# Optimization experiments

Measured on AMD Instinct MI355X. Metric: run time of the kernel, lower is better.

## Reference

```python
import jax, jax.numpy as jnp
import numpy as np

B, T = 2, 1024
V, D, H, L = 32000, 1024, 16, 8
DH = D // H  # 64
ROPE_BASE = 1000.0
EPS = 1e-6


def _rms_norm(x):
    # F.rms_norm(x, (C,), eps=1e-6)
    ms = jnp.mean(jnp.square(x), axis=-1, keepdims=True)
    return x * jax.lax.rsqrt(ms + EPS)


def _rope_tables(t_len):
    quarter = DH // 4
    inv_freq = jnp.concatenate([
        ROPE_BASE ** (-jnp.arange(quarter, dtype=jnp.float32) / quarter),
        jnp.zeros(quarter, dtype=jnp.float32),
    ])  # [DH/2]
    theta = jnp.arange(t_len, dtype=jnp.float32)[:, None] * inv_freq[None, :]  # [T, DH/2]
    return jnp.cos(theta), jnp.sin(theta)


def _apply_rope(x, cos, sin):
    # x: [B, H, T, DH]; cos/sin: [T, DH/2] broadcast to [1,1,T,DH/2]
    half = DH // 2
    x1, x2 = x[..., :half], x[..., half:]
    c = cos[None, None]
    s = sin[None, None]
    return jnp.concatenate([c * x1 - s * x2, s * x1 + c * x2], axis=-1).astype(x.dtype)


def setup_inputs() -> dict:
    key = jax.random.key(0)
    ks = jax.random.split(key, 7)
    s = 0.02
    return {
        "x_indices": jax.random.randint(ks[0], (B, T), 0, V, dtype=jnp.int32),
        "embedding": jax.random.normal(ks[1], (V, D), dtype=jnp.float32) * s,
        "Wqkv": jax.random.normal(ks[2], (L, 3 * D, D), dtype=jnp.float32) * s,
        "Wout": jax.random.normal(ks[3], (L, D, D), dtype=jnp.float32) * s,
        "W1": jax.random.normal(ks[4], (L, 4 * D, D), dtype=jnp.float32) * s,
        "W2": jax.random.normal(ks[5], (L, D, 4 * D), dtype=jnp.float32) * s,
        "lm_head": jax.random.normal(ks[6], (V, D), dtype=jnp.float32) * s,
    }


def reference(x_indices, embedding, Wqkv, Wout, W1, W2, lm_head):
    x = embedding[x_indices]  # [B, T, D]
    cos, sin = _rope_tables(T)
    causal = jnp.tril(jnp.ones((T, T), dtype=bool))  # [T, T]
    neg = jnp.finfo(x.dtype).min
    scale = 1.0 / np.sqrt(DH)

    for l in range(L):
        n = _rms_norm(x)
        qkv = jnp.einsum('btd,ed->bte', n, Wqkv[l])  # [B, T, 3D]
        qkv = qkv.reshape(B, T, 3, H, DH)
        q = jnp.transpose(qkv[:, :, 0], (0, 2, 1, 3))  # [B, H, T, DH]
        k = jnp.transpose(qkv[:, :, 1], (0, 2, 1, 3))
        v = jnp.transpose(qkv[:, :, 2], (0, 2, 1, 3))
        q = _apply_rope(q, cos, sin)
        k = _apply_rope(k, cos, sin)
        scores = jnp.einsum('bhqd,bhkd->bhqk', q, k) * scale
        scores = jnp.where(causal[None, None], scores, neg)
        attn = jax.nn.softmax(scores, axis=-1)
        ctx = jnp.einsum('bhqk,bhkd->bhqd', attn, v)
        ctx = jnp.transpose(ctx, (0, 2, 1, 3)).reshape(B, T, D)
        x = x + jnp.einsum('btd,ed->bte', ctx, Wout[l])
        n = _rms_norm(x)
        h = jnp.square(jax.nn.relu(jnp.einsum('btd,fd->btf', n, W1[l])))  # [B, T, 4D]
        x = x + jnp.einsum('btf,df->btd', h, W2[l])

    logits = jnp.einsum('btd,vd->btv', _rms_norm(x), lm_head)
    return logits.astype(jnp.float32)
```

## Files before the change

### kernel.cpp

```cpp
#include <hip/hip_runtime.h>
#include <hip/hip_bf16.h>
#include <cmath>
#include <cstdint>

#define B_  2
#define T_  1024
#define V_  32000
#define D_  1024
#define H_  16
#define L_  8
#define DH_ 64

typedef __attribute__((ext_vector_type(8))) short bf16x8;
typedef __attribute__((ext_vector_type(4))) float f32x4;

__device__ __forceinline__ ushort f2bf(float f) {
    union { float f; uint32_t u; } v; v.f = f;
    uint32_t r = v.u + 0x7FFFu + ((v.u >> 16) & 1u);
    return (ushort)(r >> 16);
}
__device__ __forceinline__ float bf2f(ushort u) {
    union { uint32_t u; float f; } v; v.u = ((uint32_t)u) << 16;
    return v.f;
}

__device__ __forceinline__ void async_copy16(const void* g, void* l) {
    __builtin_amdgcn_global_load_lds(
        (const __attribute__((address_space(1))) void*)g,
        (__attribute__((address_space(3))) void*)l, 16, 0, 0);
}

__global__ __launch_bounds__(256) void k_cast(const float4* __restrict__ in,
                                              ushort4* __restrict__ out, int n4) {
    for (int i = blockIdx.x * 256 + threadIdx.x; i < n4; i += gridDim.x * 256) {
        float4 v = in[i];
        out[i] = make_ushort4(f2bf(v.x), f2bf(v.y), f2bf(v.z), f2bf(v.w));
    }
}

__global__ void k_rope_tables(float* __restrict__ cosT, float* __restrict__ sinT) {
    int t = blockIdx.x;
    int i = threadIdx.x;
    float invf = (i < 16) ? powf(1000.0f, -(float)i / 16.0f) : 0.0f;
    float th = (float)t * invf;
    cosT[t * 32 + i] = cosf(th);
    sinT[t * 32 + i] = sinf(th);
}

__global__ __launch_bounds__(256) void k_gather(const int* __restrict__ idx,
                                                const float* __restrict__ emb,
                                                float* __restrict__ x) {
    int row = blockIdx.x;
    int id = idx[row];
    const float4* src = (const float4*)(emb + (size_t)id * D_);
    float4* dst = (float4*)(x + (size_t)row * D_);
    dst[threadIdx.x] = src[threadIdx.x];
}

__global__ __launch_bounds__(256) void k_rmsnorm(const float* __restrict__ x,
                                                 ushort* __restrict__ out) {
    int row = blockIdx.x;
    const float4* xr = (const float4*)(x + (size_t)row * D_);
    float4 v = xr[threadIdx.x];
    float ss = v.x * v.x + v.y * v.y + v.z * v.z + v.w * v.w;
    #pragma unroll
    for (int off = 1; off < 64; off <<= 1) ss += __shfl_xor(ss, off);
    __shared__ float wsum[4];
    int lane = threadIdx.x & 63, wv = threadIdx.x >> 6;
    if (lane == 0) wsum[wv] = ss;
    __syncthreads();
    float tot = wsum[0] + wsum[1] + wsum[2] + wsum[3];
    float inv = rsqrtf(tot * (1.0f / D_) + 1e-6f);
    ushort4 r = make_ushort4(f2bf(v.x * inv), f2bf(v.y * inv), f2bf(v.z * inv), f2bf(v.w * inv));
    *(ushort4*)(out + (size_t)row * D_ + threadIdx.x * 4) = r;
}

template<int BN, int EPI, bool OUTBF, bool CONVB>
__global__ __launch_bounds__(256) void k_mfma_gemm(const ushort* __restrict__ A,
                                                   const void* __restrict__ Wp,
                                                   void* __restrict__ Cp,
                                                   const float* __restrict__ Res,
                                                   const float* __restrict__ cosT,
                                                   const float* __restrict__ sinT,
                                                   int M, int N, int K) {
    constexpr int BM = 128;
    constexpr int MI = 4;
    constexpr int NI = BN / 32;
    __shared__ ushort As[2][BM][64];
    __shared__ ushort Bs[2][BN][64];
    const int tid = threadIdx.x;
    const int wid = tid >> 6, lane = tid & 63;
    const int wr = wid >> 1, wc = wid & 1;
    const int r16 = lane & 15, kc = lane >> 4;
    const int rx = (r16 & 7) << 4;
    const int srow8 = tid >> 3;
    const int sdcp = tid & 7;

    const int nwg = gridDim.x * gridDim.y;
    int orig = blockIdx.y * gridDim.x + blockIdx.x;
    int swz = (nwg & 7) ? orig : ((orig & 7) * (nwg >> 3) + (orig >> 3));
    const size_t bm = (size_t)(swz % gridDim.x) * BM;
    const size_t bn = (size_t)(swz / gridDim.x) * BN;

    auto stage = [&](int buf, int k0) {
        #pragma unroll
        for (int i = 0; i < 4; i++) {
            const int row = i * 32 + srow8;
            const ushort* g = A + (bm + row) * (size_t)K + k0 + ((sdcp ^ (row & 7)) * 8);
            async_copy16(g, (char*)As + buf * (BM * 128) + (i * 256 + tid) * 16);
        }
        if constexpr (!CONVB) {
            const ushort* Wb = (const ushort*)Wp;
            #pragma unroll
            for (int i = 0; i < BN / 32; i++) {
                const int row = i * 32 + srow8;
                const ushort* g = Wb + (bn + row) * (size_t)K + k0 + ((sdcp ^ (row & 7)) * 8);
                async_copy16(g, (char*)Bs + buf * (BN * 128) + (i * 256 + tid) * 16);
            }
        } else {
            const float* Wf = (const float*)Wp;
            #pragma unroll
            for (int i = 0; i < BN / 32; i++) {
                const int row = i * 32 + srow8;
                const float* src = Wf + (bn + row) * (size_t)K + k0 + sdcp * 8;
                float4 v0 = *(const float4*)(src);
                float4 v1 = *(const float4*)(src + 4);
                union { ushort u[8]; bf16x8 v; } tmp;
                tmp.u[0] = f2bf(v0.x); tmp.u[1] = f2bf(v0.y);
                tmp.u[2] = f2bf(v0.z); tmp.u[3] = f2bf(v0.w);
                tmp.u[4] = f2bf(v1.x); tmp.u[5] = f2bf(v1.y);
                tmp.u[6] = f2bf(v1.z); tmp.u[7] = f2bf(v1.w);
                *(bf16x8*)((char*)Bs + buf * (BN * 128) + row * 128 + ((sdcp ^ (row & 7)) << 4)) = tmp.v;
            }
        }
    };

    f32x4 acc[MI][NI];
    #pragma unroll
    for (int mi = 0; mi < MI; mi++)
        #pragma unroll
        for (int ni = 0; ni < NI; ni++) {
            f32x4 z = {0.f, 0.f, 0.f, 0.f};
            acc[mi][ni] = z;
        }

    const int KSTEPS = K >> 6;
    stage(0, 0);
    __syncthreads();
    for (int step = 0; step < KSTEPS; ++step) {
        const int cur = step & 1;
        if (step + 1 < KSTEPS) stage(cur ^ 1, (step + 1) << 6);
        #pragma unroll
        for (int kk = 0; kk < 2; kk++) {
            bf16x8 af[MI], bfr[NI];
            #pragma unroll
            for (int mi = 0; mi < MI; mi++)
                af[mi] = *(const bf16x8*)((const char*)As + cur * (BM * 128) +
                                          (wr * 64 + mi * 16 + r16) * 128 +
                                          ((kk * 64 + kc * 16) ^ rx));
            #pragma unroll
            for (int ni = 0; ni < NI; ni++)
                bfr[ni] = *(const bf16x8*)((const char*)Bs + cur * (BN * 128) +
                                           (wc * (BN / 2) + ni * 16 + r16) * 128 +
                                           ((kk * 64 + kc * 16) ^ rx));
            #pragma unroll
            for (int mi = 0; mi < MI; mi++)
                #pragma unroll
                for (int ni = 0; ni < NI; ni++)
                    acc[mi][ni] = __builtin_amdgcn_mfma_f32_16x16x32_bf16(af[mi], bfr[ni],
                                                                          acc[mi][ni], 0, 0, 0);
        }
        __syncthreads();
    }

    #pragma unroll
    for (int mi = 0; mi < MI; mi++) {
        #pragma unroll
        for (int j = 0; j < 4; j++) {
            const size_t row = bm + wr * 64 + mi * 16 + (lane >> 4) * 4 + j;
            if constexpr (EPI == 3) {
                static_assert(BN == 128, "rope epilogue assumes BN=128");
                const int sec = (int)((bn + wc * 64) >> 10);
                if (sec < 2) {
                    const int t = (int)(row & (T_ - 1));
                    #pragma unroll
                    for (int np = 0; np < 2; np++) {
                        const int i1 = np * 16 + r16;
                        float c = cosT[t * 32 + i1], s = sinT[t * 32 + i1];
                        float x1 = acc[mi][np][j], x2 = acc[mi][np + 2][j];
                        acc[mi][np][j]     = c * x1 - s * x2;
                        acc[mi][np + 2][j] = s * x1 + c * x2;
                    }
                }
            }
            #pragma unroll
            for (int ni = 0; ni < NI; ni++) {
                const size_t col = bn + wc * (BN / 2) + ni * 16 + r16;
                float v = acc[mi][ni][j];
                if constexpr (EPI == 1) v += Res[row * N + col];
                if constexpr (EPI == 2) { v = fmaxf(v, 0.f); v *= v; }
                if constexpr (OUTBF) {
                    ((ushort*)Cp)[row * N + col] = f2bf(v);
                } else if constexpr (EPI == 0) {
                    __builtin_nontemporal_store(v, (float*)Cp + row * N + col);
                } else {
                    ((float*)Cp)[row * N + col] = v;
                }
            }
        }
    }
}

__global__ __launch_bounds__(256) void k_attn_mfma(const ushort* __restrict__ qkv,
                                                   ushort* __restrict__ ctx) {
    __shared__ __align__(16) char lds[24576];
    const int tid = threadIdx.x;
    const int w = tid >> 6, lane = tid & 63;
    const int r16 = lane & 15, kc = lane >> 4;
    const int qb = blockIdx.x * 64;
    const int bh = blockIdx.y, b = bh >> 4, h = bh & 15;
    const size_t tok0 = (size_t)b * T_;
    const ushort* qg = qkv + (tok0 + qb) * (3 * D_) + h * DH_;
    const ushort* kg = qkv + tok0 * (3 * D_) + D_ + h * DH_;
    const ushort* vg = qkv + tok0 * (3 * D_) + 2 * D_ + h * DH_;
    const float SCALE_LOG2E = 0.125f * 1.44269504089f;

    #pragma unroll
    for (int i = 0; i < 2; i++) {
        int slot = i * 256 + tid;
        int row = slot >> 3, dcp = slot & 7;
        int d0 = (dcp ^ (row & 7)) * 8;
        async_copy16(qg + (size_t)row * (3 * D_) + d0, lds + 16384 + slot * 16);
    }
    __syncthreads();
    bf16x8 aq[2];
    #pragma unroll
    for (int ks = 0; ks < 2; ks++) {
        int row = w * 16 + r16;
        aq[ks] = *(const bf16x8*)(lds + 16384 + row * 128 + ((ks * 64 + kc * 16) ^ ((row & 7) << 4)));
    }

    f32x4 o[4];
    float m[4], l[4], corr[4];
    #pragma unroll
    for (int nd = 0; nd < 4; nd++) { f32x4 z = {0.f, 0.f, 0.f, 0.f}; o[nd] = z; }
    #pragma unroll
    for (int j = 0; j < 4; j++) { m[j] = -1e30f; l[j] = 0.f; }

    const int nch = (qb >> 6) + 1;
    for (int ch = 0; ch < nch; ch++) {
        const int kb = ch << 6;
        __syncthreads();
        #pragma unroll
        for (int i = 0; i < 2; i++) {
            int slot = i * 256 + tid;
            int row = slot >> 3, dcp = slot & 7;
            int d0 = (dcp ^ (row & 7)) * 8;
            async_copy16(kg + (size_t)(kb + row) * (3 * D_) + d0, lds + slot * 16);
        }
        {
            int key = tid >> 2, dbase = (tid & 3) * 16;
            const ushort* src = vg + (size_t)(kb + key) * (3 * D_) + dbase;
            bf16x8 v0 = *(const bf16x8*)(src);
            bf16x8 v1 = *(const bf16x8*)(src + 8);
            #pragma unroll
            for (int e = 0; e < 8; e++) {
                int d = dbase + e;
                *(ushort*)(lds + 8192 + d * 128 + ((key * 2) ^ ((d & 7) << 4))) = (ushort)v0[e];
                d = dbase + 8 + e;
                *(ushort*)(lds + 8192 + d * 128 + ((key * 2) ^ ((d & 7) << 4))) = (ushort)v1[e];
            }
        }
        __syncthreads();

        f32x4 s[4];
        #pragma unroll
        for (int ni = 0; ni < 4; ni++) { f32x4 z = {0.f, 0.f, 0.f, 0.f}; s[ni] = z; }
        __builtin_amdgcn_s_setprio(1);
        #pragma unroll
        for (int ks = 0; ks < 2; ks++)
            #pragma unroll
            for (int ni = 0; ni < 4; ni++) {
                int row = ni * 16 + r16;
                bf16x8 kf = *(const bf16x8*)(lds + row * 128 + ((ks * 64 + kc * 16) ^ ((row & 7) << 4)));
                s[ni] = __builtin_amdgcn_mfma_f32_16x16x32_bf16(aq[ks], kf, s[ni], 0, 0, 0);
            }
        __builtin_amdgcn_s_setprio(0);

        const bool diag = (kb == qb);
        #pragma unroll
        for (int j = 0; j < 4; j++) {
            const int qrow = qb + w * 16 + kc * 4 + j;
            #pragma unroll
            for (int ni = 0; ni < 4; ni++) {
                float v = s[ni][j] * SCALE_LOG2E;
                if (diag) { int key = kb + ni * 16 + r16; if (key > qrow) v = -1e30f; }
                s[ni][j] = v;
            }
            float t = fmaxf(fmaxf(s[0][j], s[1][j]), fmaxf(s[2][j], s[3][j]));
            #pragma unroll
            for (int off = 1; off < 16; off <<= 1) t = fmaxf(t, __shfl_xor(t, off));
            float mn = fmaxf(m[j], t);
            corr[j] = exp2f(m[j] - mn);
            m[j] = mn;
            float ps = 0.f;
            #pragma unroll
            for (int ni = 0; ni < 4; ni++) {
                float p = exp2f(s[ni][j] - mn);
                s[ni][j] = p;
                ps += p;
            }
            #pragma unroll
            for (int off = 1; off < 16; off <<= 1) ps += __shfl_xor(ps, off);
            l[j] = l[j] * corr[j] + ps;
        }
        #pragma unroll
        for (int ni = 0; ni < 4; ni++)
            #pragma unroll
            for (int j = 0; j < 4; j++) {
                int row = w * 16 + kc * 4 + j;
                *(ushort*)(lds + 16384 + row * 128 + ((ni * 32 + r16 * 2) ^ ((row & 7) << 4))) = f2bf(s[ni][j]);
            }
        #pragma unroll
        for (int nd = 0; nd < 4; nd++)
            #pragma unroll
            for (int j = 0; j < 4; j++) o[nd][j] *= corr[j];
        __builtin_amdgcn_s_setprio(1);
        #pragma unroll
        for (int ks = 0; ks < 2; ks++) {
            int prow = w * 16 + r16;
            bf16x8 pf = *(const bf16x8*)(lds + 16384 + prow * 128 + ((ks * 64 + kc * 16) ^ ((prow & 7) << 4)));
            #pragma unroll
            for (int nd = 0; nd < 4; nd++) {
                int drow = nd * 16 + r16;
                bf16x8 vf = *(const bf16x8*)(lds + 8192 + drow * 128 + ((ks * 64 + kc * 16) ^ ((drow & 7) << 4)));
                o[nd] = __builtin_amdgcn_mfma_f32_16x16x32_bf16(pf, vf, o[nd], 0, 0, 0);
            }
        }
        __builtin_amdgcn_s_setprio(0);
    }

    #pragma unroll
    for (int j = 0; j < 4; j++) {
        float inv = 1.0f / l[j];
        int row = qb + w * 16 + kc * 4 + j;
        ushort* dst = ctx + (tok0 + row) * D_ + h * DH_;
        #pragma unroll
        for (int nd = 0; nd < 4; nd++)
            dst[nd * 16 + r16] = f2bf(o[nd][j] * inv);
    }
}

extern "C" void kernel_launch(void* const* d_in, const int* in_sizes, int n_in,
                              void* d_out, int out_size, void* d_ws, size_t ws_size,
                              hipStream_t stream) {
    const int*   xi   = (const int*)d_in[0];
    const float* emb  = (const float*)d_in[1];
    const float* Wqkv = (const float*)d_in[2];
    const float* Wout = (const float*)d_in[3];
    const float* W1   = (const float*)d_in[4];
    const float* W2   = (const float*)d_in[5];
    const float* lmh  = (const float*)d_in[6];
    float* out = (float*)d_out;

    const size_t NT = (size_t)B_ * T_;
    size_t off = 0;
    auto carve = [&](size_t bytes) -> char* {
        char* r = (char*)d_ws + off;
        off += (bytes + 255) & ~(size_t)255;
        return r;
    };
    float*  xbuf = (float*)carve(NT * D_ * 4);
    ushort* qkv  = (ushort*)carve(NT * 3 * D_ * 2);
    ushort* nb   = (ushort*)carve(NT * D_ * 2);
    ushort* ctxb = (ushort*)carve(NT * D_ * 2);
    ushort* hb   = (ushort*)carve(NT * 4 * D_ * 2);
    float*  cosT = (float*)carve(T_ * 32 * 4);
    float*  sinT = (float*)carve(T_ * 32 * 4);

    const size_t nWqkv = (size_t)L_ * 3 * D_ * D_;
    const size_t nWout = (size_t)L_ * D_ * D_;
    const size_t nW1   = (size_t)L_ * 4 * D_ * D_;
    const size_t nW2   = (size_t)L_ * 4 * D_ * D_;
    const size_t nLmh  = (size_t)V_ * D_;
    ushort* WqkvB = (ushort*)carve(nWqkv * 2);
    ushort* WoutB = (ushort*)carve(nWout * 2);
    ushort* W1B   = (ushort*)carve(nW1 * 2);
    ushort* W2B   = (ushort*)carve(nW2 * 2);
    ushort* lmhB  = (ushort*)carve(nLmh * 2);
    const bool preconv = (off <= ws_size);

    if (preconv) {
        k_cast<<<dim3(2048), dim3(256), 0, stream>>>((const float4*)Wqkv, (ushort4*)WqkvB, (int)(nWqkv / 4));
        k_cast<<<dim3(2048), dim3(256), 0, stream>>>((const float4*)Wout, (ushort4*)WoutB, (int)(nWout / 4));
        k_cast<<<dim3(2048), dim3(256), 0, stream>>>((const float4*)W1,   (ushort4*)W1B,   (int)(nW1 / 4));
        k_cast<<<dim3(2048), dim3(256), 0, stream>>>((const float4*)W2,   (ushort4*)W2B,   (int)(nW2 / 4));
        k_cast<<<dim3(2048), dim3(256), 0, stream>>>((const float4*)lmh,  (ushort4*)lmhB,  (int)(nLmh / 4));
    }

#define LAUNCH_GEMM(BN, EPI, OUTBF, GX, GY, Aq, Wb16, Wf32, Cq, Rq, Mv, Nv, Kv)              \
    do {                                                                                     \
        if (preconv)                                                                         \
            k_mfma_gemm<BN, EPI, OUTBF, false><<<dim3(GX, GY), dim3(256), 0, stream>>>(      \
                (const ushort*)(Aq), (const void*)(Wb16), (void*)(Cq), (Rq), cosT, sinT,     \
                Mv, Nv, Kv);                                                                 \
        else                                                                                 \
            k_mfma_gemm<BN, EPI, OUTBF, true><<<dim3(GX, GY), dim3(256), 0, stream>>>(       \
                (const ushort*)(Aq), (const void*)(Wf32), (void*)(Cq), (Rq), cosT, sinT,     \
                Mv, Nv, Kv);                                                                 \
    } while (0)

    k_rope_tables<<<dim3(T_), dim3(32), 0, stream>>>(cosT, sinT);
    k_gather<<<dim3(NT), dim3(256), 0, stream>>>(xi, emb, xbuf);

    for (int l = 0; l < L_; l++) {
        k_rmsnorm<<<dim3(NT), dim3(256), 0, stream>>>(xbuf, nb);
        LAUNCH_GEMM(128, 3, true, 16, 24, nb,
                    WqkvB + (size_t)l * 3 * D_ * D_, Wqkv + (size_t)l * 3 * D_ * D_,
                    qkv, nullptr, (int)NT, 3 * D_, D_);
        k_attn_mfma<<<dim3(T_ / 64, B_ * H_), dim3(256), 0, stream>>>(qkv, ctxb);
        LAUNCH_GEMM(64, 1, false, 16, 16, ctxb,
                    WoutB + (size_t)l * D_ * D_, Wout + (size_t)l * D_ * D_,
                    xbuf, xbuf, (int)NT, D_, D_);
        k_rmsnorm<<<dim3(NT), dim3(256), 0, stream>>>(xbuf, nb);
        LAUNCH_GEMM(128, 2, true, 16, 32, nb,
                    W1B + (size_t)l * 4 * D_ * D_, W1 + (size_t)l * 4 * D_ * D_,
                    hb, nullptr, (int)NT, 4 * D_, D_);
        LAUNCH_GEMM(64, 1, false, 16, 16, hb,
                    W2B + (size_t)l * 4 * D_ * D_, W2 + (size_t)l * 4 * D_ * D_,
                    xbuf, xbuf, (int)NT, D_, 4 * D_);
    }
    k_rmsnorm<<<dim3(NT), dim3(256), 0, stream>>>(xbuf, nb);
    LAUNCH_GEMM(128, 0, false, 16, 250, nb, lmhB, lmh, out, nullptr, (int)NT, V_, D_);
#undef LAUNCH_GEMM
}
```

Before: 1.986 ms.

## Split attention KV range across two blocks and widen LM-head GEMM tile

Attention is split-K: each query tile's causal key chunks are divided between two blocks, which write unnormalised partial outputs and max/sum stats that a new combine kernel merges into bf16 context. This doubles the attention grid to reduce tail imbalance from causal work but adds a float partial round trip and an extra launch. The LM-head GEMM switches to BN=256 with single-buffered LDS (no prefetch overlap), and all GEMMs get a launch-bounds occupancy hint of 2 blocks per CU, which may constrain registers.

New measurement: 1.958 ms. Within noise of the previous version (-1.4%).

```diff
diff --git a/kernel.cpp b/kernel.cpp
--- a/kernel.cpp
+++ b/kernel.cpp
@@ -76,18 +76,20 @@
 }
 
 template<int BN, int EPI, bool OUTBF, bool CONVB>
-__global__ __launch_bounds__(256) void k_mfma_gemm(const ushort* __restrict__ A,
-                                                   const void* __restrict__ Wp,
-                                                   void* __restrict__ Cp,
-                                                   const float* __restrict__ Res,
-                                                   const float* __restrict__ cosT,
-                                                   const float* __restrict__ sinT,
-                                                   int M, int N, int K) {
+__global__ __launch_bounds__(256, 2) void k_mfma_gemm(const ushort* __restrict__ A,
+                                                      const void* __restrict__ Wp,
+                                                      void* __restrict__ Cp,
+                                                      const float* __restrict__ Res,
+                                                      const float* __restrict__ cosT,
+                                                      const float* __restrict__ sinT,
+                                                      int M, int N, int K) {
     constexpr int BM = 128;
     constexpr int MI = 4;
     constexpr int NI = BN / 32;
-    __shared__ ushort As[2][BM][64];
-    __shared__ ushort Bs[2][BN][64];
+    constexpr bool DBUF = (BN <= 128);
+    constexpr int NB = DBUF ? 2 : 1;
+    __shared__ ushort As[NB][BM][64];
+    __shared__ ushort Bs[NB][BN][64];
     const int tid = threadIdx.x;
     const int wid = tid >> 6, lane = tid & 63;
     const int wr = wid >> 1, wc = wid & 1;
@@ -144,23 +146,18 @@
             acc[mi][ni] = z;
         }
 
-    const int KSTEPS = K >> 6;
-    stage(0, 0);
-    __syncthreads();
-    for (int step = 0; step < KSTEPS; ++step) {
-        const int cur = step & 1;
-        if (step + 1 < KSTEPS) stage(cur ^ 1, (step + 1) << 6);
+    auto compute = [&](int buf) {
         #pragma unroll
         for (int kk = 0; kk < 2; kk++) {
             bf16x8 af[MI], bfr[NI];
             #pragma unroll
             for (int mi = 0; mi < MI; mi++)
-                af[mi] = *(const bf16x8*)((const char*)As + cur * (BM * 128) +
+                af[mi] = *(const bf16x8*)((const char*)As + buf * (BM * 128) +
                                           (wr * 64 + mi * 16 + r16) * 128 +
                                           ((kk * 64 + kc * 16) ^ rx));
             #pragma unroll
             for (int ni = 0; ni < NI; ni++)
-                bfr[ni] = *(const bf16x8*)((const char*)Bs + cur * (BN * 128) +
+                bfr[ni] = *(const bf16x8*)((const char*)Bs + buf * (BN * 128) +
                                            (wc * (BN / 2) + ni * 16 + r16) * 128 +
                                            ((kk * 64 + kc * 16) ^ rx));
             #pragma unroll
@@ -170,7 +167,25 @@
                     acc[mi][ni] = __builtin_amdgcn_mfma_f32_16x16x32_bf16(af[mi], bfr[ni],
                                                                           acc[mi][ni], 0, 0, 0);
         }
+    };
+
+    const int KSTEPS = K >> 6;
+    if constexpr (DBUF) {
+        stage(0, 0);
         __syncthreads();
+        for (int step = 0; step < KSTEPS; ++step) {
+            const int cur = step & 1;
+            if (step + 1 < KSTEPS) stage(cur ^ 1, (step + 1) << 6);
+            compute(cur);
+            __syncthreads();
+        }
+    } else {
+        for (int step = 0; step < KSTEPS; ++step) {
+            stage(0, step << 6);
+            __syncthreads();
+            compute(0);
+            __syncthreads();
+        }
     }
 
     #pragma unroll
@@ -211,33 +226,43 @@
     }
 }
 
-__global__ __launch_bounds__(256) void k_attn_mfma(const ushort* __restrict__ qkv,
-                                                   ushort* __restrict__ ctx) {
+__global__ __launch_bounds__(256) void k_attn_split(const ushort* __restrict__ qkv,
+                                                    float* __restrict__ po,
+                                                    float* __restrict__ pml) {
     __shared__ __align__(16) char lds[24576];
     const int tid = threadIdx.x;
     const int w = tid >> 6, lane = tid & 63;
     const int r16 = lane & 15, kc = lane >> 4;
-    const int qb = blockIdx.x * 64;
+    const int rx = (r16 & 7) << 4;
+    const int qt = blockIdx.x >> 1, hf = blockIdx.x & 1;
+    const int qb = qt * 64;
     const int bh = blockIdx.y, b = bh >> 4, h = bh & 15;
     const size_t tok0 = (size_t)b * T_;
-    const ushort* qg = qkv + (tok0 + qb) * (3 * D_) + h * DH_;
     const ushort* kg = qkv + tok0 * (3 * D_) + D_ + h * DH_;
     const ushort* vg = qkv + tok0 * (3 * D_) + 2 * D_ + h * DH_;
     const float SCALE_LOG2E = 0.125f * 1.44269504089f;
 
-    #pragma unroll
-    for (int i = 0; i < 2; i++) {
-        int slot = i * 256 + tid;
-        int row = slot >> 3, dcp = slot & 7;
-        int d0 = (dcp ^ (row & 7)) * 8;
-        async_copy16(qg + (size_t)row * (3 * D_) + d0, lds + 16384 + slot * 16);
+    const int nch = qt + 1;
+    const int mid = (nch + 1) >> 1;
+    const int ch0 = hf ? mid : 0;
+    const int ch1 = hf ? nch : mid;
+
+    {
+        const ushort* qg = qkv + (tok0 + qb) * (3 * D_) + h * DH_;
+        #pragma unroll
+        for (int i = 0; i < 2; i++) {
+            int slot = i * 256 + tid;
+            int row = slot >> 3, dcp = slot & 7;
+            int d0 = (dcp ^ (row & 7)) * 8;
+            async_copy16(qg + (size_t)row * (3 * D_) + d0, lds + 16384 + slot * 16);
+        }
     }
     __syncthreads();
     bf16x8 aq[2];
     #pragma unroll
     for (int ks = 0; ks < 2; ks++) {
         int row = w * 16 + r16;
-        aq[ks] = *(const bf16x8*)(lds + 16384 + row * 128 + ((ks * 64 + kc * 16) ^ ((row & 7) << 4)));
+        aq[ks] = *(const bf16x8*)(lds + 16384 + row * 128 + ((ks * 64 + kc * 16) ^ rx));
     }
 
     f32x4 o[4];
@@ -247,8 +272,7 @@
     #pragma unroll
     for (int j = 0; j < 4; j++) { m[j] = -1e30f; l[j] = 0.f; }
 
-    const int nch = (qb >> 6) + 1;
-    for (int ch = 0; ch < nch; ch++) {
+    for (int ch = ch0; ch < ch1; ch++) {
         const int kb = ch << 6;
         __syncthreads();
         #pragma unroll
@@ -282,7 +306,7 @@
             #pragma unroll
             for (int ni = 0; ni < 4; ni++) {
                 int row = ni * 16 + r16;
-                bf16x8 kf = *(const bf16x8*)(lds + row * 128 + ((ks * 64 + kc * 16) ^ ((row & 7) << 4)));
+                bf16x8 kf = *(const bf16x8*)(lds + row * 128 + ((ks * 64 + kc * 16) ^ rx));
                 s[ni] = __builtin_amdgcn_mfma_f32_16x16x32_bf16(aq[ks], kf, s[ni], 0, 0, 0);
             }
         __builtin_amdgcn_s_setprio(0);
@@ -297,10 +321,10 @@
                 if (diag) { int key = kb + ni * 16 + r16; if (key > qrow) v = -1e30f; }
                 s[ni][j] = v;
             }
-            float t = fmaxf(fmaxf(s[0][j], s[1][j]), fmaxf(s[2][j], s[3][j]));
-            #pragma unroll
-            for (int off = 1; off < 16; off <<= 1) t = fmaxf(t, __shfl_xor(t, off));
-            float mn = fmaxf(m[j], t);
+            float tmax = fmaxf(fmaxf(s[0][j], s[1][j]), fmaxf(s[2][j], s[3][j]));
+            #pragma unroll
+            for (int off = 1; off < 16; off <<= 1) tmax = fmaxf(tmax, __shfl_xor(tmax, off));
+            float mn = fmaxf(m[j], tmax);
             corr[j] = exp2f(m[j] - mn);
             m[j] = mn;
             float ps = 0.f;
@@ -329,25 +353,58 @@
         #pragma unroll
         for (int ks = 0; ks < 2; ks++) {
             int prow = w * 16 + r16;
-            bf16x8 pf = *(const bf16x8*)(lds + 16384 + prow * 128 + ((ks * 64 + kc * 16) ^ ((prow & 7) << 4)));
+            bf16x8 pf = *(const bf16x8*)(lds + 16384 + prow * 128 + ((ks * 64 + kc * 16) ^ rx));
             #pragma unroll
             for (int nd = 0; nd < 4; nd++) {
                 int drow = nd * 16 + r16;
-                bf16x8 vf = *(const bf16x8*)(lds + 8192 + drow * 128 + ((ks * 64 + kc * 16) ^ ((drow & 7) << 4)));
+                bf16x8 vf = *(const bf16x8*)(lds + 8192 + drow * 128 + ((ks * 64 + kc * 16) ^ rx));
                 o[nd] = __builtin_amdgcn_mfma_f32_16x16x32_bf16(pf, vf, o[nd], 0, 0, 0);
             }
         }
         __builtin_amdgcn_s_setprio(0);
     }
 
+    const int tix = (bh * 16 + qt) * 2 + hf;
+    float* pob = po + (size_t)tix * 4096;
     #pragma unroll
     for (int j = 0; j < 4; j++) {
-        float inv = 1.0f / l[j];
-        int row = qb + w * 16 + kc * 4 + j;
-        ushort* dst = ctx + (tok0 + row) * D_ + h * DH_;
+        const int row = w * 16 + kc * 4 + j;
         #pragma unroll
         for (int nd = 0; nd < 4; nd++)
-            dst[nd * 16 + r16] = f2bf(o[nd][j] * inv);
+            pob[row * 64 + nd * 16 + r16] = o[nd][j];
+        if (r16 == 0) {
+            pml[(size_t)tix * 128 + row * 2]     = m[j];
+            pml[(size_t)tix * 128 + row * 2 + 1] = l[j];
+        }
+    }
+}
+
+__global__ __launch_bounds__(256) void k_attn_comb(const float* __restrict__ po,
+                                                   const float* __restrict__ pml,
+                                                   ushort* __restrict__ ctx) {
+    const int qt = blockIdx.x, bh = blockIdx.y, b = bh >> 4, h = bh & 15;
+    const int t0 = (bh * 16 + qt) * 2;
+    const int row = threadIdx.x >> 2;
+    const int c0 = (threadIdx.x & 3) * 16;
+    const float m0 = pml[(size_t)t0 * 128 + row * 2];
+    const float l0 = pml[(size_t)t0 * 128 + row * 2 + 1];
+    const float m1 = pml[(size_t)(t0 + 1) * 128 + row * 2];
+    const float l1 = pml[(size_t)(t0 + 1) * 128 + row * 2 + 1];
+    const float M = fmaxf(m0, m1);
+    const float w0 = exp2f(m0 - M), w1 = exp2f(m1 - M);
+    const float inv = 1.0f / (l0 * w0 + l1 * w1);
+    const float* p0 = po + (size_t)t0 * 4096 + row * 64 + c0;
+    const float* p1 = po + (size_t)(t0 + 1) * 4096 + row * 64 + c0;
+    ushort* dst = ctx + ((size_t)b * T_ + qt * 64 + row) * D_ + h * DH_ + c0;
+    #pragma unroll
+    for (int i = 0; i < 4; i++) {
+        float4 a = *(const float4*)(p0 + i * 4);
+        float4 bb = *(const float4*)(p1 + i * 4);
+        ushort4 r = make_ushort4(f2bf((a.x * w0 + bb.x * w1) * inv),
+                                 f2bf((a.y * w0 + bb.y * w1) * inv),
+                                 f2bf((a.z * w0 + bb.z * w1) * inv),
+                                 f2bf((a.w * w0 + bb.w * w1) * inv));
+        *(ushort4*)(dst + i * 4) = r;
     }
 }
 
@@ -377,6 +434,8 @@
     ushort* hb   = (ushort*)carve(NT * 4 * D_ * 2);
     float*  cosT = (float*)carve(T_ * 32 * 4);
     float*  sinT = (float*)carve(T_ * 32 * 4);
+    float*  po   = (float*)carve((size_t)B_ * H_ * 16 * 2 * 4096 * 4);
+    float*  pml  = (float*)carve((size_t)B_ * H_ * 16 * 2 * 128 * 4);
 
     const size_t nWqkv = (size_t)L_ * 3 * D_ * D_;
     const size_t nWout = (size_t)L_ * D_ * D_;
@@ -418,7 +477,8 @@
         LAUNCH_GEMM(128, 3, true, 16, 24, nb,
                     WqkvB + (size_t)l * 3 * D_ * D_, Wqkv + (size_t)l * 3 * D_ * D_,
                     qkv, nullptr, (int)NT, 3 * D_, D_);
-        k_attn_mfma<<<dim3(T_ / 64, B_ * H_), dim3(256), 0, stream>>>(qkv, ctxb);
+        k_attn_split<<<dim3(32, B_ * H_), dim3(256), 0, stream>>>(qkv, po, pml);
+        k_attn_comb<<<dim3(16, B_ * H_), dim3(256), 0, stream>>>(po, pml, ctxb);
         LAUNCH_GEMM(64, 1, false, 16, 16, ctxb,
                     WoutB + (size_t)l * D_ * D_, Wout + (size_t)l * D_ * D_,
                     xbuf, xbuf, (int)NT, D_, D_);
@@ -431,6 +491,6 @@
                     xbuf, xbuf, (int)NT, D_, 4 * D_);
     }
     k_rmsnorm<<<dim3(NT), dim3(256), 0, stream>>>(xbuf, nb);
-    LAUNCH_GEMM(128, 0, false, 16, 250, nb, lmhB, lmh, out, nullptr, (int)NT, V_, D_);
+    LAUNCH_GEMM(256, 0, false, 16, 125, nb, lmhB, lmh, out, nullptr, (int)NT, V_, D_);
 #undef LAUNCH_GEMM
 }
```
